# Kernel tuning notes

Hardware: AMD Instinct MI355X
Metric: run time of the kernel (lower is better)

Reference implementation:

```python
import jax, jax.numpy as jnp
import numpy as np

B, C, P, L = 16, 64, 128, 16        # batch, channels, patches, patch_length
D = 256                              # d_model / inner_dim
NPF = 256                            # num_poly_feats
NRFF = 128                           # num_rff
RFF_SCALE = 1.0
POLY_DEGREES = (2, 3)                # degree used is poly_degrees[i] - 2 -> (0, 1)
FEAT_DIM = L + NRFF + NPF * len(POLY_DEGREES)  # 16 + 128 + 512 = 656


def setup_inputs() -> dict:
    key = jax.random.key(0)
    ks = jax.random.split(key, 8)
    x = jax.random.normal(ks[0], (B, C, P, L), jnp.float32)
    # nn.Linear weights are (out_features, in_features); stacked over the 2 degrees
    Wq = jax.random.normal(ks[1], (2, D, L), jnp.float32) * 0.1
    Wk = jax.random.normal(ks[2], (2, D, L), jnp.float32) * 0.1
    Wv = jax.random.normal(ks[3], (2, NPF, L), jnp.float32) * 0.1
    freq_w = RFF_SCALE * jax.random.normal(ks[4], (L, NRFF // 2), jnp.float32)
    freq_b = jax.random.normal(ks[5], (1, 1, 1, NRFF // 2), jnp.float32)
    proj_w = jax.random.normal(ks[6], (D, FEAT_DIM), jnp.float32) * 0.02
    proj_b = jax.random.normal(ks[7], (D,), jnp.float32) * 0.02
    return {"x": x, "Wq": Wq, "Wk": Wk, "Wv": Wv,
            "freq_w": freq_w, "freq_b": freq_b,
            "proj_w": proj_w, "proj_b": proj_b}


def reference(x, Wq, Wk, Wv, freq_w, freq_b, proj_w, proj_b):
    # x: (B, C, P, L) -> transpose(1,2): attention runs over the channel axis
    xt = jnp.transpose(x, (0, 2, 1, 3))  # (B, P, C, L)
    polys = []
    for i, deg in enumerate((0, 1)):     # poly_degrees[i] - 2
        xp = xt ** deg                   # deg 0 -> ones, deg 1 -> xt
        Q = jnp.einsum('bpcl,dl->bpcd', xp, Wq[i])   # (B,P,C,D)
        K = jnp.einsum('bpcl,dl->bpcd', xt, Wk[i])   # (B,P,C,D)
        V = jnp.einsum('bpcl,fl->bpcf', xt, Wv[i])   # (B,P,C,NPF)
        S = jnp.einsum('bpcd,bped->bpce', Q, K)      # (B,P,C,C) un-normalized scores
        pf = jnp.einsum('bpce,bpef->bpcf', S, V)     # (B,P,C,NPF)
        polys.append(jnp.transpose(pf, (0, 2, 1, 3)))  # back to (B,C,P,NPF)
    polyfeats = jnp.concatenate(polys, axis=-1)      # (B,C,P,2*NPF)

    wx = x @ freq_w + freq_b                          # (B,C,P,NRFF//2)
    rff = jnp.concatenate([jnp.sin(wx), jnp.cos(wx)], axis=-1)  # (B,C,P,NRFF)

    feats = jnp.concatenate([x, polyfeats, rff], axis=-1)  # (B,C,P,FEAT_DIM)
    return feats @ proj_w.T + proj_b                        # (B,C,P,D)
```

## Files before the change

### kernel.cpp

```cpp
#include <hip/hip_runtime.h>
#include <hip/hip_bf16.h>

#define WS_WK0   0
#define WS_A     16
#define WS_E0    272
#define WS_BT    4368

typedef float f32x4 __attribute__((ext_vector_type(4)));
typedef short s16x8 __attribute__((ext_vector_type(8)));
typedef short s16x4 __attribute__((ext_vector_type(4)));

static __device__ __forceinline__ short bf16b(float f) {
  __hip_bfloat16 h = __float2bfloat16(f);
  return __builtin_bit_cast(short, h);
}

__global__ __launch_bounds__(512)
void pre_kernel(const float* __restrict__ Wq, const float* __restrict__ Wk,
                const float* __restrict__ Wv, const float* __restrict__ pw,
                float* __restrict__ ws)
{
  __shared__ float lds[8448];
  const int t = threadIdx.x;
  const int blk = blockIdx.x;
  ushort* bt = (ushort*)(ws + WS_BT);

  if (blk == 0) {
    {
      const int d = t >> 1;
      const int lb = (t & 1) * 8;
      #pragma unroll
      for (int h = 0; h < 2; ++h) {
        const float4 vq = *(const float4*)(Wq + 4096 + t*8 + h*4);
        lds[(lb+h*4+0)*256 + d] = vq.x;
        lds[(lb+h*4+1)*256 + d] = vq.y;
        lds[(lb+h*4+2)*256 + d] = vq.z;
        lds[(lb+h*4+3)*256 + d] = vq.w;
        const float4 vk = *(const float4*)(Wk + 4096 + t*8 + h*4);
        lds[4096 + (lb+h*4+0)*256 + d] = vk.x;
        lds[4096 + (lb+h*4+1)*256 + d] = vk.y;
        lds[4096 + (lb+h*4+2)*256 + d] = vk.z;
        lds[4096 + (lb+h*4+3)*256 + d] = vk.w;
      }
    }
    if (t < 256) {
      float s = 0.f;
      #pragma unroll
      for (int q = 0; q < 4; ++q) {
        const float4 v = *(const float4*)(Wq + t*16 + q*4);
        s += v.x + v.y + v.z + v.w;
      }
      lds[8192 + t] = s;
    }
    __syncthreads();
    if (t < 256) {
      const int l1 = t >> 4, l2 = t & 15;
      const float* r1 = lds + l1*256;
      const float* r2 = lds + 4096 + l2*256;
      float s = 0.f;
      #pragma unroll 8
      for (int dq = 0; dq < 64; ++dq) {
        const float4 a = *(const float4*)(r1 + dq*4);
        const float4 b = *(const float4*)(r2 + dq*4);
        s += a.x*b.x + a.y*b.y + a.z*b.z + a.w*b.w;
      }
      ws[WS_A + t] = s;
    }
    if (t < 16) {
      float s = 0.f;
      for (int d = 0; d < 256; ++d) s += lds[8192 + d] * Wk[d*16 + t];
      ws[WS_WK0 + t] = s;
    }
  } else if (blk <= 16) {
    const int deg = (blk <= 8) ? 0 : 1;
    {
      const int f = t >> 1;
      const int lb = (t & 1) * 8;
      #pragma unroll
      for (int h = 0; h < 2; ++h) {
        const float4 v = *(const float4*)(Wv + deg*4096 + t*8 + h*4);
        lds[(lb+h*4+0)*256 + f] = v.x;
        lds[(lb+h*4+1)*256 + f] = v.y;
        lds[(lb+h*4+2)*256 + f] = v.z;
        lds[(lb+h*4+3)*256 + f] = v.w;
      }
    }
    __syncthreads();
    const int d = ((blk-1) & 7)*32 + (t >> 4);
    const int l = t & 15;
    const float* pr = pw + d*656 + (deg ? 272 : 16);
    const float* wv = lds + l*256;
    float s = 0.f;
    #pragma unroll 8
    for (int fq = 0; fq < 64; ++fq) {
      const float4 a = *(const float4*)(pr + fq*4);
      const float4 b = *(const float4*)(wv + fq*4);
      s += a.x*b.x + a.y*b.y + a.z*b.z + a.w*b.w;
    }
    if (deg == 0) {
      ws[WS_E0 + d*16 + l] = s;
      bt[d*160 + l] = (ushort)bf16b(pw[d*656 + l]);
    } else {
      bt[d*160 + 16 + l] = (ushort)bf16b(s);
    }
  } else {
    #pragma unroll 4
    for (int k = 0; k < 64; ++k) {
      const int d = k*4 + (t >> 7);
      const int j = t & 127;
      const float v = (j < 64) ? pw[d*656 + 528 + j] : pw[d*656 + 592 + (j-64)];
      bt[d*160 + 32 + j] = (ushort)bf16b(v);
    }
  }
}

__global__ __launch_bounds__(256, 2)
void main_kernel(const float* __restrict__ x, const float* __restrict__ fw,
                 const float* __restrict__ fb, const float* __restrict__ pw,
                 const float* __restrict__ pb, const float* __restrict__ ws,
                 float* __restrict__ out)
{
  __shared__ float XsT[16*68];
  __shared__ float fws[16*64];
  __shared__ float fbs[64];
  __shared__ float Gs[256];
  __shared__ float Ys[64*16];
  __shared__ float tls[16];
  __shared__ float c0s[256];
  __shared__ short Abf[20*64*8];

  const int t = threadIdx.x;
  const int b = blockIdx.x >> 7;
  const int p = blockIdx.x & 127;

  const int lane = t & 63, w = t >> 6;
  const int n0 = w << 6;
  const int lr = lane & 15, lq = lane >> 4;
  const int xc = t >> 2, xl0 = (t & 3) * 4;
  const ushort* BTW = (const ushort*)(ws + WS_BT);

  {
    const float4 v = *(const float4*)(x + (((b*64 + xc)*128 + p) << 4) + xl0);
    XsT[(xl0+0)*68 + xc] = v.x;
    XsT[(xl0+1)*68 + xc] = v.y;
    XsT[(xl0+2)*68 + xc] = v.z;
    XsT[(xl0+3)*68 + xc] = v.w;
    s16x4 xb;
    xb[0] = bf16b(v.x); xb[1] = bf16b(v.y); xb[2] = bf16b(v.z); xb[3] = bf16b(v.w);
    *(s16x4*)&Abf[(((xl0>>3)*64 + xc) << 3) + (xl0 & 4)] = xb;
  }
  *(float4*)(fws + t*4) = *(const float4*)(fw + t*4);
  if (t < 16) *(float4*)(fbs + t*4) = *(const float4*)(fb + t*4);
  __syncthreads();

  {
    const int l1 = t >> 4, l2 = t & 15;
    const float* r1 = XsT + l1*68;
    const float* r2 = XsT + l2*68;
    float g = 0.f;
    #pragma unroll
    for (int cq = 0; cq < 16; ++cq) {
      const float4 a = *(const float4*)(r1 + cq*4);
      const float4 bb = *(const float4*)(r2 + cq*4);
      g += a.x*bb.x + a.y*bb.y + a.z*bb.z + a.w*bb.w;
    }
    Gs[t] = g;
  }
  {
    float4 acc4 = make_float4(0.f, 0.f, 0.f, 0.f);
    #pragma unroll
    for (int l = 0; l < 16; ++l) {
      const float xv = XsT[l*68 + xc];
      const float4 a = *(const float4*)(ws + WS_A + l*16 + xl0);
      acc4.x += xv*a.x; acc4.y += xv*a.y; acc4.z += xv*a.z; acc4.w += xv*a.w;
    }
    *(float4*)(Ys + xc*16 + xl0) = acc4;
  }
  {
    const int c = t & 63, jb = t >> 6;
    float xr[16];
    #pragma unroll
    for (int l = 0; l < 16; ++l) xr[l] = XsT[l*68 + c];
    s16x8 ps[2], pc[2];
    #pragma unroll
    for (int jg = 0; jg < 4; ++jg) {
      const int j0 = jb*16 + jg*4;
      float4 wx4 = *(const float4*)(fbs + j0);
      #pragma unroll
      for (int l = 0; l < 16; ++l) {
        const float4 f = *(const float4*)(fws + l*64 + j0);
        wx4.x += xr[l]*f.x; wx4.y += xr[l]*f.y;
        wx4.z += xr[l]*f.z; wx4.w += xr[l]*f.w;
      }
      const int h = jg >> 1, e0 = (jg & 1) * 4;
      float sv, cv;
      __sincosf(wx4.x, &sv, &cv); ps[h][e0+0] = bf16b(sv); pc[h][e0+0] = bf16b(cv);
      __sincosf(wx4.y, &sv, &cv); ps[h][e0+1] = bf16b(sv); pc[h][e0+1] = bf16b(cv);
      __sincosf(wx4.z, &sv, &cv); ps[h][e0+2] = bf16b(sv); pc[h][e0+2] = bf16b(cv);
      __sincosf(wx4.w, &sv, &cv); ps[h][e0+3] = bf16b(sv); pc[h][e0+3] = bf16b(cv);
    }
    *(s16x8*)&Abf[(((4 + 2*jb)*64 + c) << 3)] = ps[0];
    *(s16x8*)&Abf[(((5 + 2*jb)*64 + c) << 3)] = ps[1];
    *(s16x8*)&Abf[(((12 + 2*jb)*64 + c) << 3)] = pc[0];
    *(s16x8*)&Abf[(((13 + 2*jb)*64 + c) << 3)] = pc[1];
  }
  __syncthreads();

  {
    float4 m = make_float4(0.f, 0.f, 0.f, 0.f);
    #pragma unroll
    for (int k = 0; k < 16; ++k) {
      const float yv = Ys[xc*16 + k];
      const float4 g = *(const float4*)(Gs + k*16 + xl0);
      m.x += yv*g.x; m.y += yv*g.y; m.z += yv*g.z; m.w += yv*g.w;
    }
    s16x4 mb;
    mb[0] = bf16b(m.x); mb[1] = bf16b(m.y); mb[2] = bf16b(m.z); mb[3] = bf16b(m.w);
    *(s16x4*)&Abf[(((2 + (xl0>>3))*64 + xc) << 3) + (xl0 & 4)] = mb;
  }
  if (t < 16) {
    float s = 0.f;
    #pragma unroll
    for (int q = 0; q < 4; ++q) {
      const float4 g = *(const float4*)(Gs + t*16 + q*4);
      const float4 wk = *(const float4*)(ws + WS_WK0 + q*4);
      s += g.x*wk.x + g.y*wk.y + g.z*wk.z + g.w*wk.w;
    }
    tls[t] = s;
  }
  __syncthreads();

  {
    float tl[16], e[16];
    #pragma unroll
    for (int q = 0; q < 4; ++q) {
      *(float4*)(tl + q*4) = *(const float4*)(tls + q*4);
      *(float4*)(e + q*4) = *(const float4*)(ws + WS_E0 + t*16 + q*4);
    }
    float s = pb[t];
    #pragma unroll
    for (int l = 0; l < 16; ++l) s += tl[l] * e[l];
    c0s[t] = s;
  }

  f32x4 acc[4][4] = {};
  #pragma unroll
  for (int ks = 0; ks < 5; ++ks) {
    s16x8 af[4], bf_[4];
    #pragma unroll
    for (int mi = 0; mi < 4; ++mi)
      af[mi] = *(const s16x8*)&Abf[(((ks*4 + lq)*64) + mi*16 + lr) << 3];
    #pragma unroll
    for (int nt = 0; nt < 4; ++nt)
      bf_[nt] = *(const s16x8*)&BTW[(n0 + nt*16 + lr)*160 + ks*32 + lq*8];
    #pragma unroll
    for (int mi = 0; mi < 4; ++mi)
      #pragma unroll
      for (int nt = 0; nt < 4; ++nt)
        acc[mi][nt] = __builtin_amdgcn_mfma_f32_16x16x32_bf16(af[mi], bf_[nt], acc[mi][nt], 0, 0, 0);
  }

  #pragma unroll
  for (int nt = 0; nt < 4; ++nt) {
    const int d = n0 + nt*16 + lr;
    const float cc = c0s[d];
    #pragma unroll
    for (int mi = 0; mi < 4; ++mi) {
      #pragma unroll
      for (int r = 0; r < 4; ++r) {
        const int c = mi*16 + lq*4 + r;
        out[(((b*64 + c)*128 + p) << 8) + d] = acc[mi][nt][r] + cc;
      }
    }
  }
}

extern "C" void kernel_launch(void* const* d_in, const int* in_sizes, int n_in,
                              void* d_out, int out_size, void* d_ws, size_t ws_size,
                              hipStream_t stream) {
  const float* x  = (const float*)d_in[0];
  const float* Wq = (const float*)d_in[1];
  const float* Wk = (const float*)d_in[2];
  const float* Wv = (const float*)d_in[3];
  const float* fw = (const float*)d_in[4];
  const float* fb = (const float*)d_in[5];
  const float* pw = (const float*)d_in[6];
  const float* pb = (const float*)d_in[7];
  float* out = (float*)d_out;
  float* ws  = (float*)d_ws;

  pre_kernel<<<18, 512, 0, stream>>>(Wq, Wk, Wv, pw, ws);
  main_kernel<<<16*128, 256, 0, stream>>>(x, fw, fb, pw, pb, ws, out);
}
```

Baseline: 55.75 us.

## Split fused kernel into activation and GEMM kernels staged through output buffer

Splits the single main kernel into an activation kernel that writes the bf16 A-operand and per-row bias into the output buffer as scratch, and a GEMM kernel that reads them back. The GEMM kernel swaps MFMA operand roles so each lane writes contiguous float4 rows of the output instead of scattered scalar stores. The activation kernel drops the large LDS tile and raises its occupancy bound, and the Wk0 reduction in the pre-kernel is parallelised. The cost is an extra kernel launch and a global round trip of the intermediates. It also depends on a barrier in the GEMM kernel to keep each block's output stores from overwriting scratch slabs before they are read.

```diff
diff --git a/kernel.cpp b/kernel.cpp
--- a/kernel.cpp
+++ b/kernel.cpp
@@ -6,6 +6,8 @@
 #define WS_E0    272
 #define WS_BT    4368
 
+#define SLAB(b,p,kt) ((((b)*64 + (kt))*128 + (p)) << 8)
+
 typedef float f32x4 __attribute__((ext_vector_type(4)));
 typedef short s16x8 __attribute__((ext_vector_type(8)));
 typedef short s16x4 __attribute__((ext_vector_type(4)));
@@ -13,6 +15,10 @@
 static __device__ __forceinline__ short bf16b(float f) {
   __hip_bfloat16 h = __float2bfloat16(f);
   return __builtin_bit_cast(short, h);
+}
+
+static __device__ __forceinline__ void bar_lds() {
+  asm volatile("s_waitcnt lgkmcnt(0)\n\ts_barrier" ::: "memory");
 }
 
 __global__ __launch_bounds__(512)
@@ -20,7 +26,7 @@
                 const float* __restrict__ Wv, const float* __restrict__ pw,
                 float* __restrict__ ws)
 {
-  __shared__ float lds[8448];
+  __shared__ float lds[8704];
   const int t = threadIdx.x;
   const int blk = blockIdx.x;
   ushort* bt = (ushort*)(ws + WS_BT);
@@ -66,9 +72,19 @@
       }
       ws[WS_A + t] = s;
     }
+    if (t < 256) {
+      const int l = t & 15, ch = t >> 4;
+      float s = 0.f;
+      #pragma unroll
+      for (int i = 0; i < 16; ++i)
+        s += lds[8192 + ch*16 + i] * Wk[(ch*16 + i)*16 + l];
+      lds[8448 + t] = s;
+    }
+    __syncthreads();
     if (t < 16) {
       float s = 0.f;
-      for (int d = 0; d < 256; ++d) s += lds[8192 + d] * Wk[d*16 + t];
+      #pragma unroll
+      for (int ch = 0; ch < 16; ++ch) s += lds[8448 + ch*16 + t];
       ws[WS_WK0 + t] = s;
     }
   } else if (blk <= 16) {
@@ -114,11 +130,10 @@
   }
 }
 
-__global__ __launch_bounds__(256, 2)
-void main_kernel(const float* __restrict__ x, const float* __restrict__ fw,
-                 const float* __restrict__ fb, const float* __restrict__ pw,
-                 const float* __restrict__ pb, const float* __restrict__ ws,
-                 float* __restrict__ out)
+__global__ __launch_bounds__(256, 4)
+void acts_kernel(const float* __restrict__ x, const float* __restrict__ fw,
+                 const float* __restrict__ fb, const float* __restrict__ pb,
+                 const float* __restrict__ ws, float* __restrict__ out)
 {
   __shared__ float XsT[16*68];
   __shared__ float fws[16*64];
@@ -126,18 +141,11 @@
   __shared__ float Gs[256];
   __shared__ float Ys[64*16];
   __shared__ float tls[16];
-  __shared__ float c0s[256];
-  __shared__ short Abf[20*64*8];
 
   const int t = threadIdx.x;
   const int b = blockIdx.x >> 7;
   const int p = blockIdx.x & 127;
-
-  const int lane = t & 63, w = t >> 6;
-  const int n0 = w << 6;
-  const int lr = lane & 15, lq = lane >> 4;
   const int xc = t >> 2, xl0 = (t & 3) * 4;
-  const ushort* BTW = (const ushort*)(ws + WS_BT);
 
   {
     const float4 v = *(const float4*)(x + (((b*64 + xc)*128 + p) << 4) + xl0);
@@ -147,11 +155,11 @@
     XsT[(xl0+3)*68 + xc] = v.w;
     s16x4 xb;
     xb[0] = bf16b(v.x); xb[1] = bf16b(v.y); xb[2] = bf16b(v.z); xb[3] = bf16b(v.w);
-    *(s16x4*)&Abf[(((xl0>>3)*64 + xc) << 3) + (xl0 & 4)] = xb;
+    *(s16x4*)((ushort*)(out + SLAB(b, p, (xl0 >> 3))) + xc*8 + (xl0 & 4)) = xb;
   }
   *(float4*)(fws + t*4) = *(const float4*)(fw + t*4);
   if (t < 16) *(float4*)(fbs + t*4) = *(const float4*)(fb + t*4);
-  __syncthreads();
+  bar_lds();
 
   {
     const int l1 = t >> 4, l2 = t & 15;
@@ -199,12 +207,12 @@
       __sincosf(wx4.z, &sv, &cv); ps[h][e0+2] = bf16b(sv); pc[h][e0+2] = bf16b(cv);
       __sincosf(wx4.w, &sv, &cv); ps[h][e0+3] = bf16b(sv); pc[h][e0+3] = bf16b(cv);
     }
-    *(s16x8*)&Abf[(((4 + 2*jb)*64 + c) << 3)] = ps[0];
-    *(s16x8*)&Abf[(((5 + 2*jb)*64 + c) << 3)] = ps[1];
-    *(s16x8*)&Abf[(((12 + 2*jb)*64 + c) << 3)] = pc[0];
-    *(s16x8*)&Abf[(((13 + 2*jb)*64 + c) << 3)] = pc[1];
-  }
-  __syncthreads();
+    *(s16x8*)((ushort*)(out + SLAB(b, p,  4 + 2*jb)) + c*8) = ps[0];
+    *(s16x8*)((ushort*)(out + SLAB(b, p,  5 + 2*jb)) + c*8) = ps[1];
+    *(s16x8*)((ushort*)(out + SLAB(b, p, 12 + 2*jb)) + c*8) = pc[0];
+    *(s16x8*)((ushort*)(out + SLAB(b, p, 13 + 2*jb)) + c*8) = pc[1];
+  }
+  bar_lds();
 
   {
     float4 m = make_float4(0.f, 0.f, 0.f, 0.f);
@@ -216,7 +224,7 @@
     }
     s16x4 mb;
     mb[0] = bf16b(m.x); mb[1] = bf16b(m.y); mb[2] = bf16b(m.z); mb[3] = bf16b(m.w);
-    *(s16x4*)&Abf[(((2 + (xl0>>3))*64 + xc) << 3) + (xl0 & 4)] = mb;
+    *(s16x4*)((ushort*)(out + SLAB(b, p, 2 + (xl0 >> 3))) + xc*8 + (xl0 & 4)) = mb;
   }
   if (t < 16) {
     float s = 0.f;
@@ -228,7 +236,7 @@
     }
     tls[t] = s;
   }
-  __syncthreads();
+  bar_lds();
 
   {
     float tl[16], e[16];
@@ -240,8 +248,20 @@
     float s = pb[t];
     #pragma unroll
     for (int l = 0; l < 16; ++l) s += tl[l] * e[l];
-    c0s[t] = s;
-  }
+    out[SLAB(b, p, 20) + t] = s;
+  }
+}
+
+__global__ __launch_bounds__(256, 2)
+void gemm_kernel(const float* __restrict__ ws, float* out)
+{
+  const int t = threadIdx.x;
+  const int b = blockIdx.x >> 7;
+  const int p = blockIdx.x & 127;
+  const int lane = t & 63, w = t >> 6;
+  const int n0 = w << 6;
+  const int lr = lane & 15, lq = lane >> 4;
+  const ushort* BTW = (const ushort*)(ws + WS_BT);
 
   f32x4 acc[4][4] = {};
   #pragma unroll
@@ -249,10 +269,10 @@
     s16x8 af[4], bf_[4];
     #pragma unroll
     for (int mi = 0; mi < 4; ++mi)
-      af[mi] = *(const s16x8*)&Abf[(((ks*4 + lq)*64) + mi*16 + lr) << 3];
+      af[mi] = *(const s16x8*)&BTW[(n0 + mi*16 + lr)*160 + ks*32 + lq*8];
     #pragma unroll
     for (int nt = 0; nt < 4; ++nt)
-      bf_[nt] = *(const s16x8*)&BTW[(n0 + nt*16 + lr)*160 + ks*32 + lq*8];
+      bf_[nt] = *(const s16x8*)((const ushort*)(out + SLAB(b, p, ks*4 + lq)) + (nt*16 + lr)*8);
     #pragma unroll
     for (int mi = 0; mi < 4; ++mi)
       #pragma unroll
@@ -260,17 +280,25 @@
         acc[mi][nt] = __builtin_amdgcn_mfma_f32_16x16x32_bf16(af[mi], bf_[nt], acc[mi][nt], 0, 0, 0);
   }
 
+  float4 cv[4];
+  #pragma unroll
+  for (int mi = 0; mi < 4; ++mi)
+    cv[mi] = *(const float4*)(out + SLAB(b, p, 20) + n0 + mi*16 + (lq << 2));
+
+  __syncthreads();
+
   #pragma unroll
   for (int nt = 0; nt < 4; ++nt) {
-    const int d = n0 + nt*16 + lr;
-    const float cc = c0s[d];
+    const int c = nt*16 + lr;
+    float* rp = out + (((b*64 + c)*128 + p) << 8) + n0 + (lq << 2);
     #pragma unroll
     for (int mi = 0; mi < 4; ++mi) {
-      #pragma unroll
-      for (int r = 0; r < 4; ++r) {
-        const int c = mi*16 + lq*4 + r;
-        out[(((b*64 + c)*128 + p) << 8) + d] = acc[mi][nt][r] + cc;
-      }
+      float4 o;
+      o.x = acc[mi][nt][0] + cv[mi].x;
+      o.y = acc[mi][nt][1] + cv[mi].y;
+      o.z = acc[mi][nt][2] + cv[mi].z;
+      o.w = acc[mi][nt][3] + cv[mi].w;
+      *(float4*)(rp + mi*16) = o;
     }
   }
 }
@@ -290,5 +318,6 @@
   float* ws  = (float*)d_ws;
 
   pre_kernel<<<18, 512, 0, stream>>>(Wq, Wk, Wv, pw, ws);
-  main_kernel<<<16*128, 256, 0, stream>>>(x, fw, fb, pw, pb, ws, out);
-}
+  acts_kernel<<<16*128, 256, 0, stream>>>(x, fw, fb, pb, ws, out);
+  gemm_kernel<<<16*128, 256, 0, stream>>>(ws, out);
+}
```

Measured after the change: 78.38 us. 40.6% more time.

## Split output columns across two blocks and reassociate poly feature product

Applied to the files above, without the earlier changes.

Doubles the main grid so each block computes half of the 256 output columns, giving each wave 32 columns instead of 64. The degree-1 poly term is reordered from (X·A)·G to X·(A·G), using a small 16x16 product that removes the 64x16 Ys buffer. A barrier that was missing before c0s is read is added, and __syncthreads is replaced by an inline-asm waitcnt plus s_barrier. The pre-kernel's serial 256-step Wk reduction becomes a two-stage parallel sum. In exchange, every block now repeats the preprocessing of its x tile (Gram, sincos RFF, poly features), which doubles that work.

```diff
diff --git a/kernel.cpp b/kernel.cpp
--- a/kernel.cpp
+++ b/kernel.cpp
@@ -13,6 +13,10 @@
 static __device__ __forceinline__ short bf16b(float f) {
   __hip_bfloat16 h = __float2bfloat16(f);
   return __builtin_bit_cast(short, h);
+}
+
+static __device__ __forceinline__ void bar_lds() {
+  asm volatile("s_waitcnt lgkmcnt(0)\n\ts_barrier" ::: "memory");
 }
 
 __global__ __launch_bounds__(512)
@@ -20,7 +24,7 @@
                 const float* __restrict__ Wv, const float* __restrict__ pw,
                 float* __restrict__ ws)
 {
-  __shared__ float lds[8448];
+  __shared__ float lds[8704];
   const int t = threadIdx.x;
   const int blk = blockIdx.x;
   ushort* bt = (ushort*)(ws + WS_BT);
@@ -66,9 +70,19 @@
       }
       ws[WS_A + t] = s;
     }
+    if (t < 256) {
+      const int l = t & 15, ch = t >> 4;
+      float s = 0.f;
+      #pragma unroll
+      for (int i = 0; i < 16; ++i)
+        s += lds[8192 + ch*16 + i] * Wk[(ch*16 + i)*16 + l];
+      lds[8448 + t] = s;
+    }
+    __syncthreads();
     if (t < 16) {
       float s = 0.f;
-      for (int d = 0; d < 256; ++d) s += lds[8192 + d] * Wk[d*16 + t];
+      #pragma unroll
+      for (int ch = 0; ch < 16; ++ch) s += lds[8448 + ch*16 + t];
       ws[WS_WK0 + t] = s;
     }
   } else if (blk <= 16) {
@@ -124,17 +138,18 @@
   __shared__ float fws[16*64];
   __shared__ float fbs[64];
   __shared__ float Gs[256];
-  __shared__ float Ys[64*16];
+  __shared__ float AGs[256];
   __shared__ float tls[16];
   __shared__ float c0s[256];
   __shared__ short Abf[20*64*8];
 
   const int t = threadIdx.x;
-  const int b = blockIdx.x >> 7;
-  const int p = blockIdx.x & 127;
+  const int b  = blockIdx.x >> 8;
+  const int p  = (blockIdx.x >> 1) & 127;
+  const int dh = blockIdx.x & 1;
 
   const int lane = t & 63, w = t >> 6;
-  const int n0 = w << 6;
+  const int n0 = dh*128 + w*32;
   const int lr = lane & 15, lq = lane >> 4;
   const int xc = t >> 2, xl0 = (t & 3) * 4;
   const ushort* BTW = (const ushort*)(ws + WS_BT);
@@ -151,7 +166,7 @@
   }
   *(float4*)(fws + t*4) = *(const float4*)(fw + t*4);
   if (t < 16) *(float4*)(fbs + t*4) = *(const float4*)(fb + t*4);
-  __syncthreads();
+  bar_lds();
 
   {
     const int l1 = t >> 4, l2 = t & 15;
@@ -165,16 +180,6 @@
       g += a.x*bb.x + a.y*bb.y + a.z*bb.z + a.w*bb.w;
     }
     Gs[t] = g;
-  }
-  {
-    float4 acc4 = make_float4(0.f, 0.f, 0.f, 0.f);
-    #pragma unroll
-    for (int l = 0; l < 16; ++l) {
-      const float xv = XsT[l*68 + xc];
-      const float4 a = *(const float4*)(ws + WS_A + l*16 + xl0);
-      acc4.x += xv*a.x; acc4.y += xv*a.y; acc4.z += xv*a.z; acc4.w += xv*a.w;
-    }
-    *(float4*)(Ys + xc*16 + xl0) = acc4;
   }
   {
     const int c = t & 63, jb = t >> 6;
@@ -204,19 +209,18 @@
     *(s16x8*)&Abf[(((12 + 2*jb)*64 + c) << 3)] = pc[0];
     *(s16x8*)&Abf[(((13 + 2*jb)*64 + c) << 3)] = pc[1];
   }
-  __syncthreads();
-
-  {
-    float4 m = make_float4(0.f, 0.f, 0.f, 0.f);
-    #pragma unroll
-    for (int k = 0; k < 16; ++k) {
-      const float yv = Ys[xc*16 + k];
-      const float4 g = *(const float4*)(Gs + k*16 + xl0);
-      m.x += yv*g.x; m.y += yv*g.y; m.z += yv*g.z; m.w += yv*g.w;
-    }
-    s16x4 mb;
-    mb[0] = bf16b(m.x); mb[1] = bf16b(m.y); mb[2] = bf16b(m.z); mb[3] = bf16b(m.w);
-    *(s16x4*)&Abf[(((2 + (xl0>>3))*64 + xc) << 3) + (xl0 & 4)] = mb;
+  bar_lds();
+
+  {
+    const int l = t >> 4, lp = t & 15;
+    float a[16];
+    #pragma unroll
+    for (int q = 0; q < 4; ++q)
+      *(float4*)(a + q*4) = *(const float4*)(ws + WS_A + l*16 + q*4);
+    float s = 0.f;
+    #pragma unroll
+    for (int k = 0; k < 16; ++k) s += a[k] * Gs[k*16 + lp];
+    AGs[t] = s;
   }
   if (t < 16) {
     float s = 0.f;
@@ -228,8 +232,20 @@
     }
     tls[t] = s;
   }
-  __syncthreads();
-
+  bar_lds();
+
+  {
+    float4 m = make_float4(0.f, 0.f, 0.f, 0.f);
+    #pragma unroll
+    for (int l = 0; l < 16; ++l) {
+      const float xv = XsT[l*68 + xc];
+      const float4 g = *(const float4*)(AGs + l*16 + xl0);
+      m.x += xv*g.x; m.y += xv*g.y; m.z += xv*g.z; m.w += xv*g.w;
+    }
+    s16x4 mb;
+    mb[0] = bf16b(m.x); mb[1] = bf16b(m.y); mb[2] = bf16b(m.z); mb[3] = bf16b(m.w);
+    *(s16x4*)&Abf[(((2 + (xl0>>3))*64 + xc) << 3) + (xl0 & 4)] = mb;
+  }
   {
     float tl[16], e[16];
     #pragma unroll
@@ -242,26 +258,27 @@
     for (int l = 0; l < 16; ++l) s += tl[l] * e[l];
     c0s[t] = s;
   }
-
-  f32x4 acc[4][4] = {};
+  bar_lds();
+
+  f32x4 acc[4][2] = {};
   #pragma unroll
   for (int ks = 0; ks < 5; ++ks) {
-    s16x8 af[4], bf_[4];
+    s16x8 af[4], bf_[2];
     #pragma unroll
     for (int mi = 0; mi < 4; ++mi)
       af[mi] = *(const s16x8*)&Abf[(((ks*4 + lq)*64) + mi*16 + lr) << 3];
     #pragma unroll
-    for (int nt = 0; nt < 4; ++nt)
+    for (int nt = 0; nt < 2; ++nt)
       bf_[nt] = *(const s16x8*)&BTW[(n0 + nt*16 + lr)*160 + ks*32 + lq*8];
     #pragma unroll
     for (int mi = 0; mi < 4; ++mi)
       #pragma unroll
-      for (int nt = 0; nt < 4; ++nt)
+      for (int nt = 0; nt < 2; ++nt)
         acc[mi][nt] = __builtin_amdgcn_mfma_f32_16x16x32_bf16(af[mi], bf_[nt], acc[mi][nt], 0, 0, 0);
   }
 
   #pragma unroll
-  for (int nt = 0; nt < 4; ++nt) {
+  for (int nt = 0; nt < 2; ++nt) {
     const int d = n0 + nt*16 + lr;
     const float cc = c0s[d];
     #pragma unroll
@@ -290,5 +307,5 @@
   float* ws  = (float*)d_ws;
 
   pre_kernel<<<18, 512, 0, stream>>>(Wq, Wk, Wv, pw, ws);
-  main_kernel<<<16*128, 256, 0, stream>>>(x, fw, fb, pw, pb, ws, out);
-}
+  main_kernel<<<16*128*2, 256, 0, stream>>>(x, fw, fb, pw, pb, ws, out);
+}
```

New measurement: 66.15 us. +18.6%, slower.
